# Performance work log

Measured on AMD Instinct MI355X. Metric: run time of the kernel, lower is better.

## Reference

```python
import jax, jax.numpy as jnp
import numpy as np

B, S, D = 4, 2048, 1024
E, H, K = 32, 128, 2


def setup_inputs() -> dict:
    key = jax.random.key(0)
    k1, k2, k3, k4 = jax.random.split(key, 4)
    scale_d = 1.0 / np.sqrt(D)
    scale_h = 1.0 / np.sqrt(H)
    return {
        "x": jax.random.normal(k1, (B, S, D), dtype=jnp.float32),
        "w_sel": jax.random.normal(k2, (E, D), dtype=jnp.float32) * scale_d,      # router Linear weight [E, D]
        "w_keys": jax.random.normal(k3, (E, D, H), dtype=jnp.float32) * scale_d,  # per-expert up-proj
        "w_values": jax.random.normal(k4, (E, H, D), dtype=jnp.float32) * scale_h, # per-expert down-proj
        "k": K,
    }


def reference(x, w_sel, w_keys, w_values, k):
    # Router: sigmoid gating + top-k expert selection per token.
    sel = jax.nn.sigmoid(jnp.einsum('bsd,ed->bse', x, w_sel))      # [B,S,E]
    sel_val, sel_idx = jax.lax.top_k(sel, k)                       # [B,S,k]
    n_exp = w_sel.shape[0]
    # Dense gate matrix: gate[b,s,e] = sum of sel_val over heads routed to e
    # (top_k indices are distinct, so this matches the per-head accumulation).
    gate = jnp.sum(jax.nn.one_hot(sel_idx, n_exp, dtype=x.dtype) * sel_val[..., None], axis=-2)  # [B,S,E]
    # Expert up-projection + ReLU for all experts (dense equivalent of the
    # per-token gathered keys[expert_idx](token); unselected experts are
    # zeroed by the gate so the math is identical).
    scores = jax.nn.relu(jnp.einsum('bsd,edh->bseh', x, w_keys))   # [B,S,E,H]
    weighted = scores * gate[..., None]                            # [B,S,E,H]
    out = jnp.einsum('bseh,ehd->bsd', weighted, w_values)          # [B,S,D]
    return out
```

## Files before the change

kernel.cpp:

```cpp
#include <hip/hip_runtime.h>
#include <cstdint>
#include <cstddef>

#define NTOK 8192
#define DIM  1024
#define NEXP 32
#define NH   128
#define TT   32
#define NSLOT 32
#define BK   128
#define RT   32
#define LCAP 1024
#define NRB  (NTOK / RT)

typedef __attribute__((ext_vector_type(8))) short short8;
typedef __attribute__((ext_vector_type(4))) float float4_;

static __device__ __forceinline__ unsigned short f2bf(float f) {
  unsigned u = __float_as_uint(f);
  return (unsigned short)((u + 0x7fffu + ((u >> 16) & 1u)) >> 16);
}
static __device__ __forceinline__ float bf2f(unsigned short h) {
  return __uint_as_float(((unsigned)h) << 16);
}
static __device__ __forceinline__ void gload_lds16(const unsigned short* g,
                                                   unsigned short* l) {
  __builtin_amdgcn_global_load_lds(
      (const __attribute__((address_space(1))) unsigned int*)(const void*)g,
      (__attribute__((address_space(3))) unsigned int*)(void*)l, 16, 0, 0);
}

__global__ __launch_bounds__(256) void prep_router_kernel(
    const float* __restrict__ x, const float* __restrict__ w_sel,
    const float* __restrict__ w_keys, const float* __restrict__ w_values,
    unsigned short* __restrict__ xbf, unsigned short* __restrict__ wk_t,
    unsigned short* __restrict__ wv_t,
    int* __restrict__ counts, unsigned* __restrict__ list)
{
  __shared__ __align__(16) char smem[22144];
  const int bid = blockIdx.x;
  const int tid = threadIdx.x;

  if (bid >= NRB) {
    float (*tile)[65] = (float (*)[65])smem;
    const int lb = bid - NRB;
    const float* src; unsigned short* dst; int R, C, e, t, tpc;
    if (lb < 1024) { src = w_keys;   dst = wk_t; R = DIM; C = NH;  e = lb >> 5;          t = lb & 31; tpc = 2; }
    else           { src = w_values; dst = wv_t; R = NH;  C = DIM; e = (lb - 1024) >> 5; t = (lb - 1024) & 31; tpc = 16; }
    const int r0 = (t / tpc) * 64;
    const int c0 = (t % tpc) * 64;
    const float* s = src + (size_t)e * R * C;
    unsigned short* d = dst + (size_t)e * R * C;

    const int i  = tid >> 2;
    const int j0 = (tid & 3) * 16;
    #pragma unroll
    for (int k4 = 0; k4 < 4; ++k4) {
      float4 v = *(const float4*)(s + (size_t)(r0 + i) * C + c0 + j0 + k4 * 4);
      tile[i][j0 + k4 * 4 + 0] = v.x;
      tile[i][j0 + k4 * 4 + 1] = v.y;
      tile[i][j0 + k4 * 4 + 2] = v.z;
      tile[i][j0 + k4 * 4 + 3] = v.w;
    }
    __syncthreads();
    unsigned pk[8];
    #pragma unroll
    for (int k = 0; k < 8; ++k) {
      unsigned lo = f2bf(tile[j0 + 2 * k][i]);
      unsigned hi = f2bf(tile[j0 + 2 * k + 1][i]);
      pk[k] = lo | (hi << 16);
    }
    uint4 u0; u0.x = pk[0]; u0.y = pk[1]; u0.z = pk[2]; u0.w = pk[3];
    uint4 u1; u1.x = pk[4]; u1.y = pk[5]; u1.z = pk[6]; u1.w = pk[7];
    unsigned short* dp = d + (size_t)(c0 + i) * R + r0 + j0;
    *(uint4*)(dp)     = u0;
    *(uint4*)(dp + 8) = u1;
    return;
  }

  float (*xs_t)[36] = (float (*)[36])smem;
  float (*ws)[68]   = (float (*)[68])(smem + 9216);
  float (*S)[33]    = (float (*)[33])(smem + 9216 + 8704);

  const int tok0 = bid * RT;
  const int tr   = tid >> 3;
  const int i8   = tid & 7;
  const int d8   = i8 * 8;
  const int tg4  = i8 * 4;
  const int swzW = i8 << 2;

  float acc[4] = {0.f, 0.f, 0.f, 0.f};

  float4 a0, a1, b0, b1;
  {
    const float* xp = x + (size_t)(tok0 + tr) * DIM + d8;
    a0 = *(const float4*)(xp);
    a1 = *(const float4*)(xp + 4);
    const float* wp = w_sel + (size_t)tr * DIM + d8;
    b0 = *(const float4*)(wp);
    b1 = *(const float4*)(wp + 4);
  }

  for (int c = 0; c < 16; ++c) {
    const int dc = c * 64;

    {
      const int colx = tr ^ swzW;
      xs_t[d8 + 0][colx] = a0.x; xs_t[d8 + 1][colx] = a0.y;
      xs_t[d8 + 2][colx] = a0.z; xs_t[d8 + 3][colx] = a0.w;
      xs_t[d8 + 4][colx] = a1.x; xs_t[d8 + 5][colx] = a1.y;
      xs_t[d8 + 6][colx] = a1.z; xs_t[d8 + 7][colx] = a1.w;
      *(float4*)&ws[tr][d8]     = b0;
      *(float4*)&ws[tr][d8 + 4] = b1;
      uint4 u;
      u.x = (unsigned)f2bf(a0.x) | ((unsigned)f2bf(a0.y) << 16);
      u.y = (unsigned)f2bf(a0.z) | ((unsigned)f2bf(a0.w) << 16);
      u.z = (unsigned)f2bf(a1.x) | ((unsigned)f2bf(a1.y) << 16);
      u.w = (unsigned)f2bf(a1.z) | ((unsigned)f2bf(a1.w) << 16);
      *(uint4*)(xbf + (size_t)(tok0 + tr) * DIM + dc + d8) = u;
    }
    __syncthreads();

    if (c < 15) {
      const float* xp = x + (size_t)(tok0 + tr) * DIM + dc + 64 + d8;
      a0 = *(const float4*)(xp);
      a1 = *(const float4*)(xp + 4);
      const float* wp = w_sel + (size_t)tr * DIM + dc + 64 + d8;
      b0 = *(const float4*)(wp);
      b1 = *(const float4*)(wp + 4);
    }

    #pragma unroll
    for (int d4 = 0; d4 < 64; d4 += 4) {
      float4 w4 = *(const float4*)&ws[tr][d4];
      const int cx = tg4 ^ ((d4 >> 3) << 2);
      float4 x0 = *(const float4*)&xs_t[d4 + 0][cx];
      float4 x1 = *(const float4*)&xs_t[d4 + 1][cx];
      float4 x2 = *(const float4*)&xs_t[d4 + 2][cx];
      float4 x3 = *(const float4*)&xs_t[d4 + 3][cx];
      acc[0] = fmaf(x0.x, w4.x, acc[0]); acc[1] = fmaf(x0.y, w4.x, acc[1]);
      acc[2] = fmaf(x0.z, w4.x, acc[2]); acc[3] = fmaf(x0.w, w4.x, acc[3]);
      acc[0] = fmaf(x1.x, w4.y, acc[0]); acc[1] = fmaf(x1.y, w4.y, acc[1]);
      acc[2] = fmaf(x1.z, w4.y, acc[2]); acc[3] = fmaf(x1.w, w4.y, acc[3]);
      acc[0] = fmaf(x2.x, w4.z, acc[0]); acc[1] = fmaf(x2.y, w4.z, acc[1]);
      acc[2] = fmaf(x2.z, w4.z, acc[2]); acc[3] = fmaf(x2.w, w4.z, acc[3]);
      acc[0] = fmaf(x3.x, w4.w, acc[0]); acc[1] = fmaf(x3.y, w4.w, acc[1]);
      acc[2] = fmaf(x3.z, w4.w, acc[2]); acc[3] = fmaf(x3.w, w4.w, acc[3]);
    }
    __syncthreads();
  }

  #pragma unroll
  for (int j = 0; j < 4; ++j)
    S[tg4 + j][tr] = acc[j];
  __syncthreads();

  if (tid < RT) {
    const int t = tid;
    float m1 = -1e30f, m2 = -1e30f;
    int i1 = 0, i2 = 0;
    for (int ee = 0; ee < NEXP; ++ee) {
      float v = S[t][ee];
      if (v > m1)      { m2 = m1; i2 = i1; m1 = v; i1 = ee; }
      else if (v > m2) { m2 = v; i2 = ee; }
    }
    const int token = tok0 + t;
    float g1 = 1.f / (1.f + __expf(-m1));
    float g2 = 1.f / (1.f + __expf(-m2));
    unsigned e1 = ((unsigned)f2bf(g1) << 16) | ((unsigned)token << 1);
    unsigned e2 = ((unsigned)f2bf(g2) << 16) | ((unsigned)token << 1) | 1u;
    int p1 = atomicAdd(&counts[i1], 1);
    if (p1 < LCAP) list[i1 * LCAP + p1] = e1;
    int p2 = atomicAdd(&counts[i2], 1);
    if (p2 < LCAP) list[i2 * LCAP + p2] = e2;
  }
}

__global__ __launch_bounds__(256, 4) void ffn_kernel(
    const unsigned short* __restrict__ xbf,
    const unsigned short* __restrict__ wk_t,
    const unsigned short* __restrict__ wv_t,
    float* __restrict__ out,
    unsigned short* __restrict__ cont,
    const int* __restrict__ counts, const unsigned* __restrict__ list,
    int use_cont)
{
  const int bid = blockIdx.x;
  const int e   = bid & 31;
  const int cnt = min(counts[e], LCAP);
  const int t0  = (bid >> 5) * TT;
  if (t0 >= cnt) return;

  __shared__ __align__(16) unsigned short uni[8448];
  __shared__ unsigned short ss[TT][NH + 8];
  __shared__ int   toks[TT];
  __shared__ float gates[TT];
  unsigned short (*xsf)[4096] = (unsigned short (*)[4096])uni;
  unsigned short (*st)[264]   = (unsigned short (*)[264])uni;

  const int tid  = threadIdx.x;
  const int wave = tid >> 6;
  const int lane = tid & 63;
  const int quad = lane >> 4;
  const int l16  = lane & 15;

  const unsigned short* wkb = wk_t + (size_t)e * NH * DIM;
  const unsigned short* wvb = wv_t + (size_t)e * DIM * NH;
  const int n_tok = min(TT, cnt - t0);

  if (tid < TT) {
    int valid = tid < n_tok;
    unsigned en = valid ? list[e * LCAP + t0 + tid] : 0u;
    toks[tid]  = valid ? (int)(en & 0xffffu) : -1;
    gates[tid] = valid ? bf2f((unsigned short)(en >> 16)) : 0.f;
  }
  __syncthreads();

  const int smt  = wave >> 1;
  const int skk0 = (wave & 1) * 2;
  {
    int sl   = toks[smt * 16 + l16];
    int gtok = (sl < 0) ? 0 : (sl >> 1);
    const unsigned short* gsrc = xbf + (size_t)gtok * DIM + quad * 8;

    #pragma unroll
    for (int i2 = 0; i2 < 2; ++i2)
      gload_lds16(gsrc + (skk0 + i2) * 32, &xsf[0][(smt * 4 + skk0 + i2) * 512]);
    __syncthreads();

    float4_ acc[2][2];
    #pragma unroll
    for (int mt = 0; mt < 2; ++mt)
      #pragma unroll
      for (int nt = 0; nt < 2; ++nt) acc[mt][nt] = (float4_){0.f, 0.f, 0.f, 0.f};

    for (int ci = 0; ci < 8; ++ci) {
      const int dc = ci * BK;
      if (ci < 7) {
        const int nb = (ci + 1) & 1;
        #pragma unroll
        for (int i2 = 0; i2 < 2; ++i2)
          gload_lds16(gsrc + dc + BK + (skk0 + i2) * 32,
                      &xsf[nb][(smt * 4 + skk0 + i2) * 512]);
      }
      short8 b[4][2];
      #pragma unroll
      for (int kk = 0; kk < 4; ++kk)
        #pragma unroll
        for (int nt = 0; nt < 2; ++nt)
          b[kk][nt] = *(const short8*)(wkb +
              (size_t)(wave * 32 + nt * 16 + l16) * DIM + dc + kk * 32 + quad * 8);

      const unsigned short* xb = &xsf[ci & 1][0];
      #pragma unroll
      for (int kk = 0; kk < 4; ++kk) {
        #pragma unroll
        for (int mt = 0; mt < 2; ++mt) {
          short8 a = *(const short8*)(xb + (mt * 4 + kk) * 512 + lane * 8);
          #pragma unroll
          for (int nt = 0; nt < 2; ++nt)
            acc[mt][nt] = __builtin_amdgcn_mfma_f32_16x16x32_bf16(a, b[kk][nt], acc[mt][nt], 0, 0, 0);
        }
      }
      __syncthreads();
    }

    #pragma unroll
    for (int mt = 0; mt < 2; ++mt)
      #pragma unroll
      for (int nt = 0; nt < 2; ++nt)
        #pragma unroll
        for (int r = 0; r < 4; ++r) {
          int row = mt * 16 + quad * 4 + r;
          float v = fmaxf(acc[mt][nt][r], 0.f) * gates[row];
          ss[row][wave * 32 + nt * 16 + l16] = f2bf(v);
        }
  }
  __syncthreads();

  #pragma unroll 1
  for (int nc = 0; nc < 4; ++nc) {
    const int colbase = wave * 256 + nc * 64;
    float4_ o[2][4];
    #pragma unroll
    for (int mt = 0; mt < 2; ++mt)
      #pragma unroll
      for (int nt = 0; nt < 4; ++nt) o[mt][nt] = (float4_){0.f, 0.f, 0.f, 0.f};

    #pragma unroll
    for (int kk = 0; kk < 4; ++kk) {
      short8 bk[4];
      #pragma unroll
      for (int nt = 0; nt < 4; ++nt)
        bk[nt] = *(const short8*)(wvb +
            (size_t)(colbase + nt * 16 + l16) * NH + kk * 32 + quad * 8);
      short8 a0 = *(const short8*)&ss[l16][kk * 32 + quad * 8];
      short8 a1 = *(const short8*)&ss[16 + l16][kk * 32 + quad * 8];
      #pragma unroll
      for (int nt = 0; nt < 4; ++nt) {
        o[0][nt] = __builtin_amdgcn_mfma_f32_16x16x32_bf16(a0, bk[nt], o[0][nt], 0, 0, 0);
        o[1][nt] = __builtin_amdgcn_mfma_f32_16x16x32_bf16(a1, bk[nt], o[1][nt], 0, 0, 0);
      }
    }

    if (use_cont) {
      #pragma unroll
      for (int mt = 0; mt < 2; ++mt)
        #pragma unroll
        for (int nt = 0; nt < 4; ++nt)
          #pragma unroll
          for (int r = 0; r < 4; ++r)
            st[mt * 16 + quad * 4 + r][wave * 64 + nt * 16 + l16] = f2bf(o[mt][nt][r]);
      __syncthreads();
      #pragma unroll
      for (int q = 0; q < 4; ++q) {
        int idx = q * 256 + tid;
        int row = idx >> 5, seg = idx & 31;
        if (row < n_tok) {
          int sl2 = toks[row];
          size_t base = ((size_t)((sl2 & 1) * NTOK + (sl2 >> 1))) * DIM
                        + (seg >> 3) * 256 + nc * 64 + (seg & 7) * 8;
          *(short8*)&cont[base] = *(const short8*)&st[row][seg * 8];
        }
      }
      __syncthreads();
    } else {
      #pragma unroll
      for (int mt = 0; mt < 2; ++mt)
        #pragma unroll
        for (int r = 0; r < 4; ++r) {
          int row = mt * 16 + quad * 4 + r;
          if (row < n_tok) {
            size_t base = (size_t)(toks[row] >> 1) * DIM + colbase;
            #pragma unroll
            for (int nt = 0; nt < 4; ++nt)
              unsafeAtomicAdd(&out[base + nt * 16 + l16], o[mt][nt][r]);
          }
        }
    }
  }
}

__global__ __launch_bounds__(256) void combine_kernel(
    const unsigned short* __restrict__ cont, float* __restrict__ out)
{
  size_t i = ((size_t)blockIdx.x * 256 + threadIdx.x) * 8;
  uint4 a = *(const uint4*)(cont + i);
  uint4 b = *(const uint4*)(cont + (size_t)NTOK * DIM + i);
  float4 r0, r1;
  r0.x = bf2f((unsigned short)(a.x & 0xffff)) + bf2f((unsigned short)(b.x & 0xffff));
  r0.y = bf2f((unsigned short)(a.x >> 16))    + bf2f((unsigned short)(b.x >> 16));
  r0.z = bf2f((unsigned short)(a.y & 0xffff)) + bf2f((unsigned short)(b.y & 0xffff));
  r0.w = bf2f((unsigned short)(a.y >> 16))    + bf2f((unsigned short)(b.y >> 16));
  r1.x = bf2f((unsigned short)(a.z & 0xffff)) + bf2f((unsigned short)(b.z & 0xffff));
  r1.y = bf2f((unsigned short)(a.z >> 16))    + bf2f((unsigned short)(b.z >> 16));
  r1.z = bf2f((unsigned short)(a.w & 0xffff)) + bf2f((unsigned short)(b.w & 0xffff));
  r1.w = bf2f((unsigned short)(a.w >> 16))    + bf2f((unsigned short)(b.w >> 16));
  *(float4*)(out + i) = r0;
  *(float4*)(out + i + 4) = r1;
}

extern "C" void kernel_launch(void* const* d_in, const int* in_sizes, int n_in,
                              void* d_out, int out_size, void* d_ws, size_t ws_size,
                              hipStream_t stream) {
  (void)in_sizes; (void)n_in;
  const float* x        = (const float*)d_in[0];
  const float* w_sel    = (const float*)d_in[1];
  const float* w_keys   = (const float*)d_in[2];
  const float* w_values = (const float*)d_in[3];
  float* out = (float*)d_out;

  char* ws = (char*)d_ws;
  size_t off = 0;
  int*            counts = (int*)(ws + off);            off += 4096;
  unsigned*       list   = (unsigned*)(ws + off);       off += (size_t)NEXP * LCAP * 4;
  unsigned short* wk_t   = (unsigned short*)(ws + off); off += (size_t)NEXP * NH * DIM * 2;
  unsigned short* wv_t   = (unsigned short*)(ws + off); off += (size_t)NEXP * NH * DIM * 2;
  unsigned short* xbf    = (unsigned short*)(ws + off); off += (size_t)NTOK * DIM * 2;
  unsigned short* cont   = (unsigned short*)(ws + off);
  size_t need_full = off + (size_t)2 * NTOK * DIM * 2;
  const int use_cont = (ws_size >= need_full) ? 1 : 0;

  hipMemsetAsync(counts, 0, NEXP * sizeof(int), stream);

  prep_router_kernel<<<NRB + 2048, 256, 0, stream>>>(x, w_sel, w_keys, w_values,
                                                     xbf, wk_t, wv_t, counts, list);

  if (!use_cont)
    hipMemsetAsync(out, 0, (size_t)out_size * sizeof(float), stream);

  ffn_kernel<<<NEXP * NSLOT, 256, 0, stream>>>(xbf, wk_t, wv_t, out, cont,
                                               counts, list, use_cont);

  if (use_cont)
    combine_kernel<<<NTOK * DIM / (256 * 8), 256, 0, stream>>>(cont, out);
}
```

Baseline: 215.4 us.

## Use 4x4 register tiles with split-K across waves in router matmul

The router GEMM inner loop moves from each thread computing 4 tokens for one expert over all 64 d-values to each thread computing a 4x4 token-by-expert tile over a 16-wide d-slice owned by its wave. The w_sel tile is now stored transposed and swizzled like x, and a final cross-wave reduction through shared memory combines the partial sums. The aim is fewer LDS reads per FMA, paid for with more accumulator registers, a larger shared buffer and an extra reduction step with a barrier.

```diff
diff --git a/kernel.cpp b/kernel.cpp
--- a/kernel.cpp
+++ b/kernel.cpp
@@ -37,7 +37,7 @@
     unsigned short* __restrict__ wv_t,
     int* __restrict__ counts, unsigned* __restrict__ list)
 {
-  __shared__ __align__(16) char smem[22144];
+  __shared__ __align__(16) char smem[22656];
   const int bid = blockIdx.x;
   const int tid = threadIdx.x;
 
@@ -79,17 +79,24 @@
   }
 
   float (*xs_t)[36] = (float (*)[36])smem;
-  float (*ws)[68]   = (float (*)[68])(smem + 9216);
-  float (*S)[33]    = (float (*)[33])(smem + 9216 + 8704);
+  float (*ws_t)[36] = (float (*)[36])(smem + 9216);
+  float (*S)[33]    = (float (*)[33])(smem + 18432);
+  float (*red)[64][16] = (float (*)[64][16])smem;
 
   const int tok0 = bid * RT;
+  const int wv   = tid >> 6;
+  const int lane = tid & 63;
   const int tr   = tid >> 3;
   const int i8   = tid & 7;
   const int d8   = i8 * 8;
-  const int tg4  = i8 * 4;
   const int swzW = i8 << 2;
-
-  float acc[4] = {0.f, 0.f, 0.f, 0.f};
+  const int tg4  = (lane & 7) * 4;
+  const int eg4  = (lane >> 3) * 4;
+  const int dlo  = wv * 16;
+
+  float acc[16];
+  #pragma unroll
+  for (int k = 0; k < 16; ++k) acc[k] = 0.f;
 
   float4 a0, a1, b0, b1;
   {
@@ -110,8 +117,10 @@
       xs_t[d8 + 2][colx] = a0.z; xs_t[d8 + 3][colx] = a0.w;
       xs_t[d8 + 4][colx] = a1.x; xs_t[d8 + 5][colx] = a1.y;
       xs_t[d8 + 6][colx] = a1.z; xs_t[d8 + 7][colx] = a1.w;
-      *(float4*)&ws[tr][d8]     = b0;
-      *(float4*)&ws[tr][d8 + 4] = b1;
+      ws_t[d8 + 0][colx] = b0.x; ws_t[d8 + 1][colx] = b0.y;
+      ws_t[d8 + 2][colx] = b0.z; ws_t[d8 + 3][colx] = b0.w;
+      ws_t[d8 + 4][colx] = b1.x; ws_t[d8 + 5][colx] = b1.y;
+      ws_t[d8 + 6][colx] = b1.z; ws_t[d8 + 7][colx] = b1.w;
       uint4 u;
       u.x = (unsigned)f2bf(a0.x) | ((unsigned)f2bf(a0.y) << 16);
       u.y = (unsigned)f2bf(a0.z) | ((unsigned)f2bf(a0.w) << 16);
@@ -131,28 +140,45 @@
     }
 
     #pragma unroll
-    for (int d4 = 0; d4 < 64; d4 += 4) {
-      float4 w4 = *(const float4*)&ws[tr][d4];
-      const int cx = tg4 ^ ((d4 >> 3) << 2);
-      float4 x0 = *(const float4*)&xs_t[d4 + 0][cx];
-      float4 x1 = *(const float4*)&xs_t[d4 + 1][cx];
-      float4 x2 = *(const float4*)&xs_t[d4 + 2][cx];
-      float4 x3 = *(const float4*)&xs_t[d4 + 3][cx];
-      acc[0] = fmaf(x0.x, w4.x, acc[0]); acc[1] = fmaf(x0.y, w4.x, acc[1]);
-      acc[2] = fmaf(x0.z, w4.x, acc[2]); acc[3] = fmaf(x0.w, w4.x, acc[3]);
-      acc[0] = fmaf(x1.x, w4.y, acc[0]); acc[1] = fmaf(x1.y, w4.y, acc[1]);
-      acc[2] = fmaf(x1.z, w4.y, acc[2]); acc[3] = fmaf(x1.w, w4.y, acc[3]);
-      acc[0] = fmaf(x2.x, w4.z, acc[0]); acc[1] = fmaf(x2.y, w4.z, acc[1]);
-      acc[2] = fmaf(x2.z, w4.z, acc[2]); acc[3] = fmaf(x2.w, w4.z, acc[3]);
-      acc[0] = fmaf(x3.x, w4.w, acc[0]); acc[1] = fmaf(x3.y, w4.w, acc[1]);
-      acc[2] = fmaf(x3.z, w4.w, acc[2]); acc[3] = fmaf(x3.w, w4.w, acc[3]);
+    for (int dd = 0; dd < 16; ++dd) {
+      const int d  = dlo + dd;
+      const int sz = (d >> 3) << 2;
+      float4 xv = *(const float4*)&xs_t[d][tg4 ^ sz];
+      float4 w4 = *(const float4*)&ws_t[d][eg4 ^ sz];
+      acc[0]  = fmaf(w4.x, xv.x, acc[0]);  acc[1]  = fmaf(w4.x, xv.y, acc[1]);
+      acc[2]  = fmaf(w4.x, xv.z, acc[2]);  acc[3]  = fmaf(w4.x, xv.w, acc[3]);
+      acc[4]  = fmaf(w4.y, xv.x, acc[4]);  acc[5]  = fmaf(w4.y, xv.y, acc[5]);
+      acc[6]  = fmaf(w4.y, xv.z, acc[6]);  acc[7]  = fmaf(w4.y, xv.w, acc[7]);
+      acc[8]  = fmaf(w4.z, xv.x, acc[8]);  acc[9]  = fmaf(w4.z, xv.y, acc[9]);
+      acc[10] = fmaf(w4.z, xv.z, acc[10]); acc[11] = fmaf(w4.z, xv.w, acc[11]);
+      acc[12] = fmaf(w4.w, xv.x, acc[12]); acc[13] = fmaf(w4.w, xv.y, acc[13]);
+      acc[14] = fmaf(w4.w, xv.z, acc[14]); acc[15] = fmaf(w4.w, xv.w, acc[15]);
     }
     __syncthreads();
   }
 
   #pragma unroll
-  for (int j = 0; j < 4; ++j)
-    S[tg4 + j][tr] = acc[j];
+  for (int ei = 0; ei < 4; ++ei) {
+    float4 v; v.x = acc[ei * 4 + 0]; v.y = acc[ei * 4 + 1];
+    v.z = acc[ei * 4 + 2]; v.w = acc[ei * 4 + 3];
+    *(float4*)&red[wv][lane][ei * 4] = v;
+  }
+  __syncthreads();
+
+  {
+    const int eg2 = tid >> 5, tg2 = (tid >> 2) & 7, ei2 = tid & 3;
+    const int cls = eg2 * 8 + tg2;
+    float4 s4; s4.x = 0.f; s4.y = 0.f; s4.z = 0.f; s4.w = 0.f;
+    #pragma unroll
+    for (int w = 0; w < 4; ++w) {
+      float4 v = *(const float4*)&red[w][cls][ei2 * 4];
+      s4.x += v.x; s4.y += v.y; s4.z += v.z; s4.w += v.w;
+    }
+    S[tg2 * 4 + 0][eg2 * 4 + ei2] = s4.x;
+    S[tg2 * 4 + 1][eg2 * 4 + ei2] = s4.y;
+    S[tg2 * 4 + 2][eg2 * 4 + ei2] = s4.z;
+    S[tg2 * 4 + 3][eg2 * 4 + ei2] = s4.w;
+  }
   __syncthreads();
 
   if (tid < RT) {
```

Result: no change. 212.2 us, median of 4 (-1.5%).

## Halve router tokens per block and split the d-reduction across waves

Applied to the files above, without the earlier changes.

The router blocks now handle 16 tokens instead of 32, which doubles the number of router blocks. Inside each block, the 64-wide d chunk is split across the four waves, each covering 16 d values, and the per-wave partial sums for experts and tokens are combined through an LDS reduction. The w_sel tile is now stored transposed with a swizzle, and each thread computes a 4-token by 2-expert tile. The aim is more parallelism and a cheaper inner loop for the router stage. The cost is that w_sel is reloaded twice as often overall, plus an extra reduction and barrier.

```diff
diff --git a/kernel.cpp b/kernel.cpp
--- a/kernel.cpp
+++ b/kernel.cpp
@@ -9,9 +9,10 @@
 #define TT   32
 #define NSLOT 32
 #define BK   128
-#define RT   32
+#define RT   16
 #define LCAP 1024
 #define NRB  (NTOK / RT)
+#define NTRB 2048
 
 typedef __attribute__((ext_vector_type(8))) short short8;
 typedef __attribute__((ext_vector_type(4))) float float4_;
@@ -37,7 +38,7 @@
     unsigned short* __restrict__ wv_t,
     int* __restrict__ counts, unsigned* __restrict__ list)
 {
-  __shared__ __align__(16) char smem[22144];
+  __shared__ __align__(16) char smem[16640];
   const int bid = blockIdx.x;
   const int tid = threadIdx.x;
 
@@ -78,24 +79,35 @@
     return;
   }
 
-  float (*xs_t)[36] = (float (*)[36])smem;
-  float (*ws)[68]   = (float (*)[68])(smem + 9216);
-  float (*S)[33]    = (float (*)[33])(smem + 9216 + 8704);
+  float (*xs_t)[20] = (float (*)[20])smem;
+  float (*ws_t)[36] = (float (*)[36])(smem + 5120);
+  float (*S)[33]    = (float (*)[33])(smem + 5120 + 9216);
+  float (*red)[16][33] = (float (*)[16][33])smem;
 
   const int tok0 = bid * RT;
+  const int wv   = tid >> 6;
+  const int lane = tid & 63;
+
+  const int tr2  = tid >> 4;
+  const int d16c = (tid & 15) * 4;
   const int tr   = tid >> 3;
   const int i8   = tid & 7;
   const int d8   = i8 * 8;
-  const int tg4  = i8 * 4;
   const int swzW = i8 << 2;
 
-  float acc[4] = {0.f, 0.f, 0.f, 0.f};
-
-  float4 a0, a1, b0, b1;
+  const int tg4  = (lane & 3) * 4;
+  const int eg2  = (lane >> 2) * 2;
+  const int dlo  = wv * 16;
+
+  const int sxw  = ((((d16c) >> 2) ^ ((d16c) >> 4)) & 3) << 2;
+
+  float acc[8];
+  #pragma unroll
+  for (int k = 0; k < 8; ++k) acc[k] = 0.f;
+
+  float4 a0, b0, b1;
   {
-    const float* xp = x + (size_t)(tok0 + tr) * DIM + d8;
-    a0 = *(const float4*)(xp);
-    a1 = *(const float4*)(xp + 4);
+    a0 = *(const float4*)(x + (size_t)(tok0 + tr2) * DIM + d16c);
     const float* wp = w_sel + (size_t)tr * DIM + d8;
     b0 = *(const float4*)(wp);
     b1 = *(const float4*)(wp + 4);
@@ -105,54 +117,63 @@
     const int dc = c * 64;
 
     {
-      const int colx = tr ^ swzW;
-      xs_t[d8 + 0][colx] = a0.x; xs_t[d8 + 1][colx] = a0.y;
-      xs_t[d8 + 2][colx] = a0.z; xs_t[d8 + 3][colx] = a0.w;
-      xs_t[d8 + 4][colx] = a1.x; xs_t[d8 + 5][colx] = a1.y;
-      xs_t[d8 + 6][colx] = a1.z; xs_t[d8 + 7][colx] = a1.w;
-      *(float4*)&ws[tr][d8]     = b0;
-      *(float4*)&ws[tr][d8 + 4] = b1;
-      uint4 u;
+      const int colx = tr2 ^ sxw;
+      xs_t[d16c + 0][colx] = a0.x; xs_t[d16c + 1][colx] = a0.y;
+      xs_t[d16c + 2][colx] = a0.z; xs_t[d16c + 3][colx] = a0.w;
+      const int colw = tr ^ swzW;
+      ws_t[d8 + 0][colw] = b0.x; ws_t[d8 + 1][colw] = b0.y;
+      ws_t[d8 + 2][colw] = b0.z; ws_t[d8 + 3][colw] = b0.w;
+      ws_t[d8 + 4][colw] = b1.x; ws_t[d8 + 5][colw] = b1.y;
+      ws_t[d8 + 6][colw] = b1.z; ws_t[d8 + 7][colw] = b1.w;
+      uint2 u;
       u.x = (unsigned)f2bf(a0.x) | ((unsigned)f2bf(a0.y) << 16);
       u.y = (unsigned)f2bf(a0.z) | ((unsigned)f2bf(a0.w) << 16);
-      u.z = (unsigned)f2bf(a1.x) | ((unsigned)f2bf(a1.y) << 16);
-      u.w = (unsigned)f2bf(a1.z) | ((unsigned)f2bf(a1.w) << 16);
-      *(uint4*)(xbf + (size_t)(tok0 + tr) * DIM + dc + d8) = u;
+      *(uint2*)(xbf + (size_t)(tok0 + tr2) * DIM + dc + d16c) = u;
     }
     __syncthreads();
 
     if (c < 15) {
-      const float* xp = x + (size_t)(tok0 + tr) * DIM + dc + 64 + d8;
-      a0 = *(const float4*)(xp);
-      a1 = *(const float4*)(xp + 4);
+      a0 = *(const float4*)(x + (size_t)(tok0 + tr2) * DIM + dc + 64 + d16c);
       const float* wp = w_sel + (size_t)tr * DIM + dc + 64 + d8;
       b0 = *(const float4*)(wp);
       b1 = *(const float4*)(wp + 4);
     }
 
     #pragma unroll
-    for (int d4 = 0; d4 < 64; d4 += 4) {
-      float4 w4 = *(const float4*)&ws[tr][d4];
-      const int cx = tg4 ^ ((d4 >> 3) << 2);
-      float4 x0 = *(const float4*)&xs_t[d4 + 0][cx];
-      float4 x1 = *(const float4*)&xs_t[d4 + 1][cx];
-      float4 x2 = *(const float4*)&xs_t[d4 + 2][cx];
-      float4 x3 = *(const float4*)&xs_t[d4 + 3][cx];
-      acc[0] = fmaf(x0.x, w4.x, acc[0]); acc[1] = fmaf(x0.y, w4.x, acc[1]);
-      acc[2] = fmaf(x0.z, w4.x, acc[2]); acc[3] = fmaf(x0.w, w4.x, acc[3]);
-      acc[0] = fmaf(x1.x, w4.y, acc[0]); acc[1] = fmaf(x1.y, w4.y, acc[1]);
-      acc[2] = fmaf(x1.z, w4.y, acc[2]); acc[3] = fmaf(x1.w, w4.y, acc[3]);
-      acc[0] = fmaf(x2.x, w4.z, acc[0]); acc[1] = fmaf(x2.y, w4.z, acc[1]);
-      acc[2] = fmaf(x2.z, w4.z, acc[2]); acc[3] = fmaf(x2.w, w4.z, acc[3]);
-      acc[0] = fmaf(x3.x, w4.w, acc[0]); acc[1] = fmaf(x3.y, w4.w, acc[1]);
-      acc[2] = fmaf(x3.z, w4.w, acc[2]); acc[3] = fmaf(x3.w, w4.w, acc[3]);
+    for (int dd = 0; dd < 16; ++dd) {
+      const int d  = dlo + dd;
+      const int sx = ((((d) >> 2) ^ ((d) >> 4)) & 3) << 2;
+      const int sw = (d >> 3) << 2;
+      float4 xv = *(const float4*)&xs_t[d][tg4 ^ sx];
+      float2 w2 = *(const float2*)&ws_t[d][eg2 ^ sw];
+      acc[0] = fmaf(w2.x, xv.x, acc[0]);
+      acc[1] = fmaf(w2.x, xv.y, acc[1]);
+      acc[2] = fmaf(w2.x, xv.z, acc[2]);
+      acc[3] = fmaf(w2.x, xv.w, acc[3]);
+      acc[4] = fmaf(w2.y, xv.x, acc[4]);
+      acc[5] = fmaf(w2.y, xv.y, acc[5]);
+      acc[6] = fmaf(w2.y, xv.z, acc[6]);
+      acc[7] = fmaf(w2.y, xv.w, acc[7]);
     }
     __syncthreads();
   }
 
   #pragma unroll
-  for (int j = 0; j < 4; ++j)
-    S[tg4 + j][tr] = acc[j];
+  for (int k = 0; k < 2; ++k)
+    #pragma unroll
+    for (int j = 0; j < 4; ++j)
+      red[wv][tg4 + j][eg2 + k] = acc[k * 4 + j];
+  __syncthreads();
+
+  {
+    #pragma unroll
+    for (int h = 0; h < 2; ++h) {
+      const int o   = h * 256 + tid;
+      const int tok = o & 15, ee = o >> 4;
+      S[tok][ee] = red[0][tok][ee] + red[1][tok][ee]
+                 + red[2][tok][ee] + red[3][tok][ee];
+    }
+  }
   __syncthreads();
 
   if (tid < RT) {
@@ -383,7 +404,7 @@
 
   hipMemsetAsync(counts, 0, NEXP * sizeof(int), stream);
 
-  prep_router_kernel<<<NRB + 2048, 256, 0, stream>>>(x, w_sel, w_keys, w_values,
+  prep_router_kernel<<<NRB + NTRB, 256, 0, stream>>>(x, w_sel, w_keys, w_values,
                                                      xbf, wk_t, wv_t, counts, list);
 
   if (!use_cont)
```

After: 214.2 us. About the same (-0.5%).
